# Kernel optimization log

Measured on AMD Instinct MI355X. Metric: run time of the kernel, lower is better.

## Reference

```python
import jax, jax.numpy as jnp
import numpy as np

NUM_HEADS = 12
SEQ_H = 32
SEQ_W = 32
D_HALF = 32
ROPE_BASE = 10000.0
LN_EPS = 1e-5


def build_rope_cache(seq_len, head_dim, base=ROPE_BASE):
    inv_freq = 1.0 / base ** (jnp.arange(0, head_dim, 2, dtype=jnp.float32) / head_dim)
    t = jnp.arange(seq_len, dtype=jnp.float32)
    freqs = jnp.outer(t, inv_freq)  # [seq_len, head_dim//2]
    cos = jnp.repeat(jnp.cos(freqs), 2, axis=-1)  # [seq_len, head_dim]
    sin = jnp.repeat(jnp.sin(freqs), 2, axis=-1)
    return cos, sin


def apply_rope(x, cos, sin):
    # x: [B,H,N,d_sub], cos/sin: [N,d_sub]
    x_even, x_odd = x[..., ::2], x[..., 1::2]
    x_rot = jnp.stack([-x_odd, x_even], axis=-1).reshape(x.shape)
    return x * cos[None, None] + x_rot * sin[None, None]


def setup_inputs() -> dict:
    key = jax.random.key(0)
    ks = jax.random.split(key, 3)
    B, N, D = 8, 1025, 768
    return {
        "x": jax.random.normal(ks[0], (B, N, D), dtype=jnp.float32),
        "ln_g": jnp.ones((D,), dtype=jnp.float32),
        "ln_b": jnp.zeros((D,), dtype=jnp.float32),
        "w_qkv": jax.random.normal(ks[1], (3 * D, D), dtype=jnp.float32) * 0.02,
        "w_proj": jax.random.normal(ks[2], (D, D), dtype=jnp.float32) * 0.02,
        "b_proj": jnp.zeros((D,), dtype=jnp.float32),
    }


def reference(x, ln_g, ln_b, w_qkv, w_proj, b_proj):
    B, N, D = x.shape
    H = NUM_HEADS
    hd = D // H
    d2 = D_HALF
    scale = hd ** -0.5

    # LayerNorm
    mu = jnp.mean(x, axis=-1, keepdims=True)
    var = jnp.mean(jnp.square(x - mu), axis=-1, keepdims=True)
    xn = (x - mu) * jax.lax.rsqrt(var + LN_EPS) * ln_g + ln_b

    # QKV projection (no bias)
    qkv = jnp.einsum("bnd,ed->bne", xn, w_qkv).reshape(B, N, 3, H, hd)
    qkv = jnp.transpose(qkv, (2, 0, 3, 1, 4))  # [3,B,H,N,hd]
    q, k, v = qkv[0], qkv[1], qkv[2]

    # 2D position ids (CLS token -> row 0, col 0)
    patch_lin = jnp.arange(N - 1)
    rows = patch_lin // SEQ_W
    cols = patch_lin % SEQ_W
    zero = jnp.zeros((1,), dtype=patch_lin.dtype)
    row_ids = jnp.concatenate([zero, rows])
    col_ids = jnp.concatenate([zero, cols])

    cos_row, sin_row = build_rope_cache(SEQ_H, d2)
    cos_col, sin_col = build_rope_cache(SEQ_W, d2)
    cos_r, sin_r = cos_row[row_ids], sin_row[row_ids]  # [N,d2]
    cos_c, sin_c = cos_col[col_ids], sin_col[col_ids]

    q = jnp.concatenate(
        [apply_rope(q[..., :d2], cos_r, sin_r), apply_rope(q[..., d2:], cos_c, sin_c)], axis=-1)
    k = jnp.concatenate(
        [apply_rope(k[..., :d2], cos_r, sin_r), apply_rope(k[..., d2:], cos_c, sin_c)], axis=-1)

    attn = jnp.einsum("bhqd,bhkd->bhqk", q, k) * scale
    attn = jax.nn.softmax(attn, axis=-1)
    out = jnp.einsum("bhqk,bhkd->bhqd", attn, v)  # [B,H,N,hd]
    out = jnp.transpose(out, (0, 2, 1, 3)).reshape(B, N, D)
    return jnp.einsum("bnd,ed->bne", out, w_proj) + b_proj
```

## Files before the change

### kernel.cpp

```cpp
#include <hip/hip_runtime.h>
#include <hip/hip_bf16.h>

typedef unsigned short u16;

#define B_      8
#define N_      1025
#define D_      768
#define H_      12
#define HD_     64
#define M_REAL  (B_ * N_)
#define M_PAD   8320
#define QKVC    (3 * D_)

typedef __attribute__((ext_vector_type(8))) short bf16x8;
typedef __attribute__((ext_vector_type(4))) float f32x4;

static __device__ __forceinline__ float bf2f(u16 u) {
    union { unsigned int i; float f; } v; v.i = ((unsigned int)u) << 16; return v.f;
}
static __device__ __forceinline__ u16 f2bf(float f) {
    union { float f; unsigned int i; } v; v.f = f;
    unsigned int x = v.i;
    return (u16)((x + 0x7fffu + ((x >> 16) & 1u)) >> 16);
}
static __device__ __forceinline__ unsigned int fbits(float f) {
    union { float f; unsigned int i; } v; v.f = f; return v.i;
}

static __device__ __forceinline__ void g2l16(const u16* g, u16* l) {
    __builtin_amdgcn_global_load_lds(
        (const __attribute__((address_space(1))) unsigned int*)g,
        (__attribute__((address_space(3))) unsigned int*)l, 16, 0, 0);
}

__global__ __launch_bounds__(256)
void ln_f2b_kernel(const float* __restrict__ x, const float* __restrict__ g,
                   const float* __restrict__ bvec, u16* __restrict__ xn,
                   const float* __restrict__ wq, u16* __restrict__ wqb,
                   const float* __restrict__ wp, u16* __restrict__ wpb)
{
    const int tid = threadIdx.x;
    if (blockIdx.x >= M_REAL) {
        int i = (blockIdx.x - M_REAL) * 1024 + tid * 4;
        const float* src; u16* dst;
        if (i < QKVC * D_) { src = wq + i; dst = wqb + i; }
        else { src = wp + (i - QKVC * D_); dst = wpb + (i - QKVC * D_); }
        float4 v = *(const float4*)src;
        dst[0] = f2bf(v.x); dst[1] = f2bf(v.y);
        dst[2] = f2bf(v.z); dst[3] = f2bf(v.w);
        return;
    }
    const int row = blockIdx.x;
    const float* xr = x + (size_t)row * D_;
    float v[3];
    float s = 0.f, ss = 0.f;
#pragma unroll
    for (int j = 0; j < 3; j++) {
        float val = xr[tid + j * 256];
        v[j] = val; s += val; ss += val * val;
    }
    __shared__ float r1[256], r2[256];
    r1[tid] = s; r2[tid] = ss; __syncthreads();
    for (int off = 128; off > 0; off >>= 1) {
        if (tid < off) { r1[tid] += r1[tid + off]; r2[tid] += r2[tid + off]; }
        __syncthreads();
    }
    const float mean = r1[0] * (1.0f / D_);
    const float var  = r2[0] * (1.0f / D_) - mean * mean;
    const float rs   = rsqrtf(var + 1e-5f);
    u16* outr = xn + (size_t)row * D_;
#pragma unroll
    for (int j = 0; j < 3; j++) {
        int c = tid + j * 256;
        outr[c] = f2bf((v[j] - mean) * rs * g[c] + bvec[c]);
    }
}

template <typename OutT, bool ROPE>
__global__ __launch_bounds__(256)
void gemm_bt(const u16* __restrict__ A, const u16* __restrict__ B,
             OutT* __restrict__ C, const float* __restrict__ bias,
             int M_real, int Ncols, int K,
             int BM, int BN, int gh, int gw, int PC)
{
    const int l   = blockIdx.x;
    const int xcd = l & 7;
    const int i0  = l >> 3;
    const int pr  = xcd / PC, pc = xcd % PC;
    const int bm  = pr * gh + (i0 % gh);
    const int bn  = pc * gw + (i0 / gh);
    if (bm >= BM || bn >= BN) return;

    __shared__ __align__(16) unsigned char smem[34816];
    u16* As0 = (u16*)smem;
    u16* Bs0 = (u16*)(smem + 8192);
    u16*   ep16 = (u16*)smem;
    float* ep32 = (float*)smem;

    const int tid  = threadIdx.x;
    const int wave = tid >> 6, lane = tid & 63;
    const int wm   = (wave >> 1) * 64, wn = (wave & 1) * 64;
    const int lrow = lane & 15, lq = lane >> 4;
    const int lrow4 = lane >> 2, lchunk = lane & 3;

    int ar0 = bm * 128 + wave * 16 + lrow4;       if (ar0 >= M_real) ar0 = M_real - 1;
    int ar1 = bm * 128 + (wave + 4) * 16 + lrow4; if (ar1 >= M_real) ar1 = M_real - 1;
    const u16* apg0 = A + (size_t)ar0 * K + lchunk * 8;
    const u16* apg1 = A + (size_t)ar1 * K + lchunk * 8;
    const u16* bpg0 = B + (size_t)(bn * 128 + wave * 16 + lrow4) * K + lchunk * 8;
    const u16* bpg1 = B + (size_t)(bn * 128 + (wave + 4) * 16 + lrow4) * K + lchunk * 8;
    u16* asl0 = As0 + wave * 512;       u16* asl1 = As0 + (wave + 4) * 512;
    u16* bsl0 = Bs0 + wave * 512;       u16* bsl1 = Bs0 + (wave + 4) * 512;
    const int bufoff = 8192;

    f32x4 acc[4][4];
#pragma unroll
    for (int i = 0; i < 4; i++)
#pragma unroll
        for (int j = 0; j < 4; j++)
            acc[i][j] = (f32x4){0.f, 0.f, 0.f, 0.f};

    g2l16(apg0, asl0); g2l16(apg1, asl1);
    g2l16(bpg0, bsl0); g2l16(bpg1, bsl1);

    const int kTiles = K / 32;
    for (int kt = 0; kt < kTiles; kt++) {
        const int cur = kt & 1;
        __syncthreads();
        if (kt + 1 < kTiles) {
            const int k1 = (kt + 1) * 32;
            const int no = (cur ^ 1) * bufoff;
            g2l16(apg0 + k1, asl0 + no); g2l16(apg1 + k1, asl1 + no);
            g2l16(bpg0 + k1, bsl0 + no); g2l16(bpg1 + k1, bsl1 + no);
        }
        const u16* Asr = As0 + cur * bufoff;
        const u16* Bsr = Bs0 + cur * bufoff;
        bf16x8 af[4], bfr[4];
#pragma unroll
        for (int i = 0; i < 4; i++) {
            af[i]  = *(const bf16x8*)&Asr[(wm + i * 16 + lrow) * 32 + lq * 8];
            bfr[i] = *(const bf16x8*)&Bsr[(wn + i * 16 + lrow) * 32 + lq * 8];
        }
#pragma unroll
        for (int i = 0; i < 4; i++)
#pragma unroll
            for (int j = 0; j < 4; j++)
                acc[i][j] = __builtin_amdgcn_mfma_f32_16x16x32_bf16(af[i], bfr[j], acc[i][j], 0, 0, 0);
    }
    __syncthreads();

    if constexpr (sizeof(OutT) == 2) {
#pragma unroll
        for (int j = 0; j < 4; j++) {
            int gcol = bn * 128 + wn + j * 16 + lrow;
            float bv = bias ? bias[gcol] : 0.f;
            int qk = gcol / D_;
            int dh = gcol & 63;
            int half = dh >> 5, ii = (dh & 31) >> 1;
            float sgn = (dh & 1) ? 1.f : -1.f;
            float invf = exp2f(-(float)ii * 0.8304820237218406f);
#pragma unroll
            for (int i = 0; i < 4; i++)
#pragma unroll
                for (int r = 0; r < 4; r++) {
                    int grow = bm * 128 + wm + i * 16 + lq * 4 + r;
                    float val = acc[i][j][r] + bv;
                    if constexpr (ROPE) {
                        if (qk < 2) {
                            float partner = __shfl_xor(val, 1);
                            int n = grow % N_;
                            int pl = n - 1;
                            int pos = (n == 0) ? 0 : (half ? (pl & 31) : (pl >> 5));
                            float ang = (float)pos * invf;
                            val = val * __cosf(ang) + sgn * partner * __sinf(ang);
                        }
                    }
                    ep16[(wm + i * 16 + lq * 4 + r) * 136 + wn + j * 16 + lrow] = f2bf(val);
                }
        }
        __syncthreads();
#pragma unroll
        for (int c = 0; c < 8; c++) {
            int idx = tid + c * 256;
            int row = idx >> 4, l16 = idx & 15;
            int grow = bm * 128 + row;
            if (grow < M_real)
                *(uint4*)((u16*)C + (size_t)grow * Ncols + bn * 128 + l16 * 8) =
                    *(const uint4*)&ep16[row * 136 + l16 * 8];
        }
    } else {
#pragma unroll
        for (int s = 0; s < 2; s++) {
            if (s) __syncthreads();
            if (wm == s * 64) {
#pragma unroll
                for (int j = 0; j < 4; j++) {
                    int gcol = bn * 128 + wn + j * 16 + lrow;
                    float bv = bias ? bias[gcol] : 0.f;
#pragma unroll
                    for (int i = 0; i < 4; i++)
#pragma unroll
                        for (int r = 0; r < 4; r++)
                            ep32[(i * 16 + lq * 4 + r) * 132 + wn + j * 16 + lrow] =
                                acc[i][j][r] + bv;
                }
            }
            __syncthreads();
#pragma unroll
            for (int c = 0; c < 8; c++) {
                int idx = tid + c * 256;
                int row = idx >> 5, l32 = idx & 31;
                int grow = bm * 128 + s * 64 + row;
                if (grow < M_real)
                    *(uint4*)((float*)C + (size_t)grow * Ncols + bn * 128 + l32 * 4) =
                        *(const uint4*)&ep32[row * 132 + l32 * 4];
            }
        }
    }
}

__global__ __launch_bounds__(256)
void attn_mfma(const u16* __restrict__ qkv, u16* __restrict__ out)
{
    __shared__ __align__(16) u16 Kt[64][72];
    __shared__ __align__(16) u16 Vt[64][72];
    __shared__ __align__(16) u16 Ps[4][32][72];
    __shared__ float Lw[4][32];

    const int l   = blockIdx.x;
    const int xcd = l & 7;
    const int j0  = l >> 3;
    const int bh  = xcd * 12 + j0 / 9;
    const int b  = bh / H_, h = bh % H_;
    const int q0 = (j0 % 9) * 128;
    const int tid  = threadIdx.x;
    const int wave = tid >> 6, lane = tid & 63;
    const int lm = lane & 15, lq = lane >> 4;
    const int qw = q0 + wave * 32;

    bf16x8 qf[2][2];
#pragma unroll
    for (int sq = 0; sq < 2; sq++) {
        int qrow = qw + sq * 16 + lm; if (qrow > N_ - 1) qrow = N_ - 1;
        const u16* qptr = qkv + (size_t)(b * N_ + qrow) * QKVC + h * HD_;
        bf16x8 t0 = *(const bf16x8*)(qptr + lq * 8);
        bf16x8 t1 = *(const bf16x8*)(qptr + 32 + lq * 8);
#pragma unroll
        for (int j = 0; j < 8; j++) {
            t0[j] = (short)f2bf(bf2f((u16)t0[j]) * 0.125f);
            t1[j] = (short)f2bf(bf2f((u16)t1[j]) * 0.125f);
        }
        qf[sq][0] = t0; qf[sq][1] = t1;
    }

    float l_r[2] = {0.f, 0.f};
    f32x4 o_acc[2][4];
#pragma unroll
    for (int sq = 0; sq < 2; sq++)
#pragma unroll
        for (int t = 0; t < 4; t++)
            o_acc[sq][t] = (f32x4){0.f, 0.f, 0.f, 0.f};

    bf16x8 kreg[2], vreg[2];
    {
        int krow = lane; if (krow > N_ - 1) krow = N_ - 1;
        const u16* kvp = qkv + (size_t)(b * N_ + krow) * QKVC + h * HD_;
#pragma unroll
        for (int p = 0; p < 2; p++) {
            int dg = wave + p * 4;
            kreg[p] = *(const bf16x8*)(kvp + D_ + dg * 8);
            vreg[p] = *(const bf16x8*)(kvp + 2 * D_ + dg * 8);
        }
    }

    const int kTiles = (N_ + 63) / 64;
    for (int kt = 0; kt < kTiles; kt++) {
        const int kbase = kt * 64;
        __syncthreads();
#pragma unroll
        for (int p = 0; p < 2; p++) {
            int dg = wave + p * 4;
            *(bf16x8*)&Kt[lane][dg * 8] = kreg[p];
#pragma unroll
            for (int j = 0; j < 8; j++) Vt[dg * 8 + j][lane] = (u16)vreg[p][j];
        }
        __syncthreads();

        if (kt + 1 < kTiles) {
            int krow = kbase + 64 + lane; if (krow > N_ - 1) krow = N_ - 1;
            const u16* kvp = qkv + (size_t)(b * N_ + krow) * QKVC + h * HD_;
#pragma unroll
            for (int p = 0; p < 2; p++) {
                int dg = wave + p * 4;
                kreg[p] = *(const bf16x8*)(kvp + D_ + dg * 8);
                vreg[p] = *(const bf16x8*)(kvp + 2 * D_ + dg * 8);
            }
        }

        f32x4 sc[2][4];
#pragma unroll
        for (int st = 0; st < 4; st++) {
            bf16x8 kf0 = *(const bf16x8*)&Kt[st * 16 + lm][lq * 8];
            bf16x8 kf1 = *(const bf16x8*)&Kt[st * 16 + lm][32 + lq * 8];
#pragma unroll
            for (int sq = 0; sq < 2; sq++) {
                f32x4 s4 = (f32x4){0.f, 0.f, 0.f, 0.f};
                s4 = __builtin_amdgcn_mfma_f32_16x16x32_bf16(kf0, qf[sq][0], s4, 0, 0, 0);
                s4 = __builtin_amdgcn_mfma_f32_16x16x32_bf16(kf1, qf[sq][1], s4, 0, 0, 0);
                sc[sq][st] = s4;
            }
        }

#pragma unroll
        for (int st = 0; st < 4; st++) {
            int keyb = kbase + st * 16 + lq * 4;
#pragma unroll
            for (int sq = 0; sq < 2; sq++) {
                unsigned int u[4];
#pragma unroll
                for (int r = 0; r < 4; r++) {
                    float p = (keyb + r < N_) ? __expf(sc[sq][st][r]) : 0.f;
                    l_r[sq] += p;
                    u[r] = fbits(p) + 0x8000u;
                }
                uint2 pk;
                pk.x = (u[0] >> 16) | (u[1] & 0xffff0000u);
                pk.y = (u[2] >> 16) | (u[3] & 0xffff0000u);
                *(uint2*)&Ps[wave][sq * 16 + lm][st * 16 + lq * 4] = pk;
            }
        }
        asm volatile("s_waitcnt lgkmcnt(0)" ::: "memory");

        bf16x8 pa[2][2];
#pragma unroll
        for (int sq = 0; sq < 2; sq++) {
            pa[sq][0] = *(const bf16x8*)&Ps[wave][sq * 16 + lm][lq * 8];
            pa[sq][1] = *(const bf16x8*)&Ps[wave][sq * 16 + lm][32 + lq * 8];
        }
#pragma unroll
        for (int nt = 0; nt < 4; nt++) {
            bf16x8 vb0 = *(const bf16x8*)&Vt[nt * 16 + lm][lq * 8];
            bf16x8 vb1 = *(const bf16x8*)&Vt[nt * 16 + lm][32 + lq * 8];
#pragma unroll
            for (int sq = 0; sq < 2; sq++) {
                o_acc[sq][nt] = __builtin_amdgcn_mfma_f32_16x16x32_bf16(pa[sq][0], vb0, o_acc[sq][nt], 0, 0, 0);
                o_acc[sq][nt] = __builtin_amdgcn_mfma_f32_16x16x32_bf16(pa[sq][1], vb1, o_acc[sq][nt], 0, 0, 0);
            }
        }
    }

#pragma unroll
    for (int sq = 0; sq < 2; sq++) {
        float l2 = l_r[sq];
        l2 += __shfl_xor(l2, 16);
        l2 += __shfl_xor(l2, 32);
        if (lq == 0) Lw[wave][sq * 16 + lm] = l2;
    }
    asm volatile("s_waitcnt lgkmcnt(0)" ::: "memory");

#pragma unroll
    for (int sq = 0; sq < 2; sq++)
#pragma unroll
        for (int r = 0; r < 4; r++) {
            int q = qw + sq * 16 + lq * 4 + r;
            if (q < N_) {
                float inv = 1.0f / Lw[wave][sq * 16 + lq * 4 + r];
                u16* orow = out + (size_t)(b * N_ + q) * D_ + h * HD_ + lm;
#pragma unroll
                for (int nt = 0; nt < 4; nt++)
                    orow[nt * 16] = f2bf(o_acc[sq][nt][r] * inv);
            }
        }
}

extern "C" void kernel_launch(void* const* d_in, const int* in_sizes, int n_in,
                              void* d_out, int out_size, void* d_ws, size_t ws_size,
                              hipStream_t stream)
{
    const float* x      = (const float*)d_in[0];
    const float* ln_g   = (const float*)d_in[1];
    const float* ln_b   = (const float*)d_in[2];
    const float* w_qkv  = (const float*)d_in[3];
    const float* w_proj = (const float*)d_in[4];
    const float* b_proj = (const float*)d_in[5];

    u16* wqkv_b  = (u16*)d_ws;
    u16* wproj_b = wqkv_b + (size_t)QKVC * D_;
    u16* xn      = wproj_b + (size_t)D_ * D_;
    u16* qkv     = xn + (size_t)M_PAD * D_;
    u16* attno   = xn;

    ln_f2b_kernel<<<M_REAL + (QKVC * D_ + D_ * D_) / 1024, 256, 0, stream>>>(
        x, ln_g, ln_b, xn, w_qkv, wqkv_b, w_proj, wproj_b);

    gemm_bt<u16, true><<<1224, 256, 0, stream>>>(
        xn, wqkv_b, qkv, nullptr, M_REAL, QKVC, D_,
        65, 18, 17, 9, 2);

    attn_mfma<<<864, 256, 0, stream>>>(qkv, attno);

    gemm_bt<float, false><<<432, 256, 0, stream>>>(
        attno, wproj_b, (float*)d_out, b_proj, M_REAL, D_, D_,
        65, 6, 9, 6, 1);
}
```

Measured before the change: 221.7 us.

## Keep K and P in registers, double-buffer V tile, fold Q scale into GEMM

The attention kernel now loads K fragments straight from global memory into registers instead of staging them in LDS. It packs softmax probabilities directly into MFMA operand registers with v_cvt_pk_bf16_f32, which removes the P round-trip through shared memory. V is double-buffered in LDS with a permuted column index, so each iteration needs one barrier instead of two, and s_setprio is raised around the MFMA blocks. The 1/sqrt(d) query scale moves into the QKV GEMM epilogue, and the key mask is applied only on the last tile. The risks are more register pressure and uncoalesced per-lane K loads.

```diff
diff --git a/kernel.cpp b/kernel.cpp
--- a/kernel.cpp
+++ b/kernel.cpp
@@ -23,8 +23,10 @@
     unsigned int x = v.i;
     return (u16)((x + 0x7fffu + ((x >> 16) & 1u)) >> 16);
 }
-static __device__ __forceinline__ unsigned int fbits(float f) {
-    union { float f; unsigned int i; } v; v.f = f; return v.i;
+static __device__ __forceinline__ unsigned int cvtpk(float a, float b) {
+    unsigned int r;
+    asm volatile("v_cvt_pk_bf16_f32 %0, %1, %2" : "=v"(r) : "v"(a), "v"(b));
+    return r;
 }
 
 static __device__ __forceinline__ void g2l16(const u16* g, u16* l) {
@@ -173,6 +175,7 @@
                             int pos = (n == 0) ? 0 : (half ? (pl & 31) : (pl >> 5));
                             float ang = (float)pos * invf;
                             val = val * __cosf(ang) + sgn * partner * __sinf(ang);
+                            if (qk == 0) val *= 0.125f;
                         }
                     }
                     ep16[(wm + i * 16 + lq * 4 + r) * 136 + wn + j * 16 + lrow] = f2bf(val);
@@ -222,9 +225,7 @@
 __global__ __launch_bounds__(256)
 void attn_mfma(const u16* __restrict__ qkv, u16* __restrict__ out)
 {
-    __shared__ __align__(16) u16 Kt[64][72];
-    __shared__ __align__(16) u16 Vt[64][72];
-    __shared__ __align__(16) u16 Ps[4][32][72];
+    __shared__ __align__(16) u16 Vt[2][64][72];
     __shared__ float Lw[4][32];
 
     const int l   = blockIdx.x;
@@ -238,20 +239,19 @@
     const int lm = lane & 15, lq = lane >> 4;
     const int qw = q0 + wave * 32;
 
+    const int vcol = (lane & 35) | ((lane & 12) << 1) | ((lane & 16) >> 2);
+
     bf16x8 qf[2][2];
 #pragma unroll
     for (int sq = 0; sq < 2; sq++) {
         int qrow = qw + sq * 16 + lm; if (qrow > N_ - 1) qrow = N_ - 1;
         const u16* qptr = qkv + (size_t)(b * N_ + qrow) * QKVC + h * HD_;
-        bf16x8 t0 = *(const bf16x8*)(qptr + lq * 8);
-        bf16x8 t1 = *(const bf16x8*)(qptr + 32 + lq * 8);
-#pragma unroll
-        for (int j = 0; j < 8; j++) {
-            t0[j] = (short)f2bf(bf2f((u16)t0[j]) * 0.125f);
-            t1[j] = (short)f2bf(bf2f((u16)t1[j]) * 0.125f);
-        }
-        qf[sq][0] = t0; qf[sq][1] = t1;
-    }
+        qf[sq][0] = *(const bf16x8*)(qptr + lq * 8);
+        qf[sq][1] = *(const bf16x8*)(qptr + 32 + lq * 8);
+    }
+
+    const u16* kb_ptr = qkv + (size_t)b * N_ * QKVC + D_ + h * HD_ + lq * 8;
+    const u16* vb_ptr = qkv + (size_t)b * N_ * QKVC + 2 * D_ + h * HD_ + wave * 8;
 
     float l_r[2] = {0.f, 0.f};
     f32x4 o_acc[2][4];
@@ -261,92 +261,104 @@
         for (int t = 0; t < 4; t++)
             o_acc[sq][t] = (f32x4){0.f, 0.f, 0.f, 0.f};
 
-    bf16x8 kreg[2], vreg[2];
+    bf16x8 kf[4][2], vreg[2];
+#pragma unroll
+    for (int st = 0; st < 4; st++) {
+        const u16* p = kb_ptr + (size_t)(st * 16 + lm) * QKVC;
+        kf[st][0] = *(const bf16x8*)p;
+        kf[st][1] = *(const bf16x8*)(p + 32);
+    }
     {
-        int krow = lane; if (krow > N_ - 1) krow = N_ - 1;
-        const u16* kvp = qkv + (size_t)(b * N_ + krow) * QKVC + h * HD_;
-#pragma unroll
-        for (int p = 0; p < 2; p++) {
-            int dg = wave + p * 4;
-            kreg[p] = *(const bf16x8*)(kvp + D_ + dg * 8);
-            vreg[p] = *(const bf16x8*)(kvp + 2 * D_ + dg * 8);
-        }
+        const u16* p = vb_ptr + (size_t)lane * QKVC;
+        vreg[0] = *(const bf16x8*)p;
+        vreg[1] = *(const bf16x8*)(p + 32);
     }
 
     const int kTiles = (N_ + 63) / 64;
     for (int kt = 0; kt < kTiles; kt++) {
         const int kbase = kt * 64;
-        __syncthreads();
-#pragma unroll
-        for (int p = 0; p < 2; p++) {
-            int dg = wave + p * 4;
-            *(bf16x8*)&Kt[lane][dg * 8] = kreg[p];
-#pragma unroll
-            for (int j = 0; j < 8; j++) Vt[dg * 8 + j][lane] = (u16)vreg[p][j];
-        }
-        __syncthreads();
-
-        if (kt + 1 < kTiles) {
-            int krow = kbase + 64 + lane; if (krow > N_ - 1) krow = N_ - 1;
-            const u16* kvp = qkv + (size_t)(b * N_ + krow) * QKVC + h * HD_;
-#pragma unroll
-            for (int p = 0; p < 2; p++) {
-                int dg = wave + p * 4;
-                kreg[p] = *(const bf16x8*)(kvp + D_ + dg * 8);
-                vreg[p] = *(const bf16x8*)(kvp + 2 * D_ + dg * 8);
-            }
+        const int buf = kt & 1;
+
+#pragma unroll
+        for (int pp = 0; pp < 2; pp++) {
+            int dg = wave + pp * 4;
+#pragma unroll
+            for (int j = 0; j < 8; j++)
+                Vt[buf][dg * 8 + j][vcol] = (u16)vreg[pp][j];
         }
 
         f32x4 sc[2][4];
-#pragma unroll
-        for (int st = 0; st < 4; st++) {
-            bf16x8 kf0 = *(const bf16x8*)&Kt[st * 16 + lm][lq * 8];
-            bf16x8 kf1 = *(const bf16x8*)&Kt[st * 16 + lm][32 + lq * 8];
+        __builtin_amdgcn_s_setprio(1);
+#pragma unroll
+        for (int st = 0; st < 4; st++)
 #pragma unroll
             for (int sq = 0; sq < 2; sq++) {
                 f32x4 s4 = (f32x4){0.f, 0.f, 0.f, 0.f};
-                s4 = __builtin_amdgcn_mfma_f32_16x16x32_bf16(kf0, qf[sq][0], s4, 0, 0, 0);
-                s4 = __builtin_amdgcn_mfma_f32_16x16x32_bf16(kf1, qf[sq][1], s4, 0, 0, 0);
+                s4 = __builtin_amdgcn_mfma_f32_16x16x32_bf16(kf[st][0], qf[sq][0], s4, 0, 0, 0);
+                s4 = __builtin_amdgcn_mfma_f32_16x16x32_bf16(kf[st][1], qf[sq][1], s4, 0, 0, 0);
                 sc[sq][st] = s4;
             }
-        }
-
-#pragma unroll
-        for (int st = 0; st < 4; st++) {
-            int keyb = kbase + st * 16 + lq * 4;
-#pragma unroll
-            for (int sq = 0; sq < 2; sq++) {
-                unsigned int u[4];
-#pragma unroll
-                for (int r = 0; r < 4; r++) {
-                    float p = (keyb + r < N_) ? __expf(sc[sq][st][r]) : 0.f;
-                    l_r[sq] += p;
-                    u[r] = fbits(p) + 0x8000u;
+        __builtin_amdgcn_s_setprio(0);
+
+        if (kt + 1 < kTiles) {
+            const int kb = kbase + 64;
+#pragma unroll
+            for (int st = 0; st < 4; st++) {
+                int kr = kb + st * 16 + lm; if (kr > N_ - 1) kr = N_ - 1;
+                const u16* p = kb_ptr + (size_t)kr * QKVC;
+                kf[st][0] = *(const bf16x8*)p;
+                kf[st][1] = *(const bf16x8*)(p + 32);
+            }
+            int kr = kb + lane; if (kr > N_ - 1) kr = N_ - 1;
+            const u16* p = vb_ptr + (size_t)kr * QKVC;
+            vreg[0] = *(const bf16x8*)p;
+            vreg[1] = *(const bf16x8*)(p + 32);
+        }
+
+        asm volatile("s_waitcnt lgkmcnt(0)" ::: "memory");
+        __builtin_amdgcn_s_barrier();
+
+        const bool lastT = (kt == kTiles - 1);
+        bf16x8 pa[2][2];
+#pragma unroll
+        for (int sq = 0; sq < 2; sq++) {
+            union { bf16x8 v; unsigned int u[4]; } pk0, pk1;
+#pragma unroll
+            for (int st = 0; st < 4; st++) {
+                float p0 = __expf(sc[sq][st][0]);
+                float p1 = __expf(sc[sq][st][1]);
+                float p2 = __expf(sc[sq][st][2]);
+                float p3 = __expf(sc[sq][st][3]);
+                if (lastT) {
+                    const int keyb = kbase + st * 16 + lq * 4;
+                    if (keyb + 0 >= N_) p0 = 0.f;
+                    if (keyb + 1 >= N_) p1 = 0.f;
+                    if (keyb + 2 >= N_) p2 = 0.f;
+                    if (keyb + 3 >= N_) p3 = 0.f;
                 }
-                uint2 pk;
-                pk.x = (u[0] >> 16) | (u[1] & 0xffff0000u);
-                pk.y = (u[2] >> 16) | (u[3] & 0xffff0000u);
-                *(uint2*)&Ps[wave][sq * 16 + lm][st * 16 + lq * 4] = pk;
-            }
-        }
-        asm volatile("s_waitcnt lgkmcnt(0)" ::: "memory");
-
-        bf16x8 pa[2][2];
-#pragma unroll
-        for (int sq = 0; sq < 2; sq++) {
-            pa[sq][0] = *(const bf16x8*)&Ps[wave][sq * 16 + lm][lq * 8];
-            pa[sq][1] = *(const bf16x8*)&Ps[wave][sq * 16 + lm][32 + lq * 8];
-        }
+                l_r[sq] += (p0 + p1) + (p2 + p3);
+                unsigned int lo = cvtpk(p0, p1);
+                unsigned int hi = cvtpk(p2, p3);
+                if      (st == 0) { pk0.u[0] = lo; pk0.u[1] = hi; }
+                else if (st == 1) { pk0.u[2] = lo; pk0.u[3] = hi; }
+                else if (st == 2) { pk1.u[0] = lo; pk1.u[1] = hi; }
+                else              { pk1.u[2] = lo; pk1.u[3] = hi; }
+            }
+            pa[sq][0] = pk0.v; pa[sq][1] = pk1.v;
+        }
+
+        __builtin_amdgcn_s_setprio(1);
 #pragma unroll
         for (int nt = 0; nt < 4; nt++) {
-            bf16x8 vb0 = *(const bf16x8*)&Vt[nt * 16 + lm][lq * 8];
-            bf16x8 vb1 = *(const bf16x8*)&Vt[nt * 16 + lm][32 + lq * 8];
+            bf16x8 vb0 = *(const bf16x8*)&Vt[buf][nt * 16 + lm][lq * 8];
+            bf16x8 vb1 = *(const bf16x8*)&Vt[buf][nt * 16 + lm][32 + lq * 8];
 #pragma unroll
             for (int sq = 0; sq < 2; sq++) {
                 o_acc[sq][nt] = __builtin_amdgcn_mfma_f32_16x16x32_bf16(pa[sq][0], vb0, o_acc[sq][nt], 0, 0, 0);
                 o_acc[sq][nt] = __builtin_amdgcn_mfma_f32_16x16x32_bf16(pa[sq][1], vb1, o_acc[sq][nt], 0, 0, 0);
             }
         }
+        __builtin_amdgcn_s_setprio(0);
     }
 
 #pragma unroll
```

After: 247.0 us. 1.11x slower.
